# Optimization experiments

Hardware: AMD Instinct MI355X
Metric: run time of the kernel (lower is better)

The kernel has to match this reference:

```python
import jax, jax.numpy as jnp
import numpy as np

ALPHA = 0.2  # LeakyReLU negative slope
N, IN_DIM, OUT_DIM = 8192, 512, 64


def setup_inputs() -> dict:
    key = jax.random.key(0)
    k1, k2, k3, k4 = jax.random.split(key, 4)
    X = jax.random.normal(k1, (N, IN_DIM), dtype=jnp.float32)
    Adj = jax.random.randint(k2, (N, N), 0, 2, dtype=jnp.int32)
    # xavier_uniform with gain=1.414
    def xavier(k, shape, gain=1.414):
        fan_in, fan_out = shape[0], shape[1]
        bound = gain * np.sqrt(6.0 / (fan_in + fan_out))
        return jax.random.uniform(k, shape, jnp.float32, -bound, bound)
    W = xavier(k3, (IN_DIM, OUT_DIM))
    a = xavier(k4, (2 * OUT_DIM, 1))
    return {"X": X, "Adj": Adj, "W": W, "a": a}


def reference(X, Adj, W, a):
    # h = X @ W : [N, D]
    h = X @ W
    D = h.shape[1]
    # Decompose pairwise score: concat([h_i, h_j]) @ a == h_i @ a1 + h_j @ a2
    s1 = h @ a[:D, 0]   # [N] -- contribution of row (destination) node i
    s2 = h @ a[D:, 0]   # [N] -- contribution of column (source) node j
    e = jnp.exp(jax.nn.leaky_relu(s1[:, None] + s2[None, :], negative_slope=ALPHA))  # [N, N]
    e = jnp.where(Adj == 0, jnp.float32(0.0), e)
    attention = e / jnp.sum(e, axis=1, keepdims=True)
    # dropout is a no-op in eval mode (training=False)
    return attention @ h
```

## Files before the change

kernel.cpp:

```cpp
#include <hip/hip_runtime.h>
#include <math.h>


#define NN 8192
#define KIN 512
#define DD 64
#define ALPHA 0.2f

using floatx4 = __attribute__((ext_vector_type(4))) float;
using bf16x8  = __attribute__((ext_vector_type(8))) __bf16;

__global__ __launch_bounds__(256) void k_fused(const float* __restrict__ X,
                                               const float* __restrict__ W,
                                               const float* __restrict__ a,
                                               float* __restrict__ s1,
                                               float* __restrict__ s2,
                                               __bf16* __restrict__ hFrag) {
    __shared__ __align__(16) float smem[3200];
    float* XT = smem;
    float* WL = smem + 32 * 36;
    float* hT = smem;
    const int t = threadIdx.x;
    const int i0 = blockIdx.x * 32;
    const int rb = t >> 5;
    const int db = t & 31;
    float acc[4][2] = {};

    for (int k0 = 0; k0 < KIN; k0 += 32) {
        {
            const int row = t >> 3, kq = t & 7;
            const float4 x4 = *(const float4*)(X + (size_t)(i0 + row) * KIN + k0 + kq * 4);
            XT[(kq * 4 + 0) * 36 + row] = x4.x;
            XT[(kq * 4 + 1) * 36 + row] = x4.y;
            XT[(kq * 4 + 2) * 36 + row] = x4.z;
            XT[(kq * 4 + 3) * 36 + row] = x4.w;
#pragma unroll
            for (int p = 0; p < 2; ++p) {
                const int q = p * 256 + t;
                const int kk = q >> 4, dq = q & 15;
                *(float4*)(WL + kk * 64 + dq * 4) =
                    *(const float4*)(W + (size_t)(k0 + kk) * DD + dq * 4);
            }
        }
        __syncthreads();
#pragma unroll
        for (int k = 0; k < 32; ++k) {
            const float4 xa = *(const float4*)(XT + k * 36 + rb * 4);
            const float2 wb = *(const float2*)(WL + k * 64 + db * 2);
            const float xv[4] = {xa.x, xa.y, xa.z, xa.w};
#pragma unroll
            for (int i = 0; i < 4; ++i) {
                acc[i][0] += xv[i] * wb.x;
                acc[i][1] += xv[i] * wb.y;
            }
        }
        __syncthreads();
    }
#pragma unroll
    for (int i = 0; i < 4; ++i) {
        hT[(rb * 4 + i) * 66 + db * 2 + 0] = acc[i][0];
        hT[(rb * 4 + i) * 66 + db * 2 + 1] = acc[i][1];
    }
    __syncthreads();
    {
        const int r = t >> 3, sub = t & 7;
        float p1 = 0.f, p2 = 0.f;
#pragma unroll
        for (int u = 0; u < 8; ++u) {
            const int d = sub * 8 + u;
            const float v = hT[r * 66 + d];
            p1 += v * a[d];
            p2 += v * a[64 + d];
        }
#pragma unroll
        for (int off = 1; off < 8; off <<= 1) {
            p1 += __shfl_xor(p1, off, 64);
            p2 += __shfl_xor(p2, off, 64);
        }
        if (sub == 0) {
            s1[i0 + r] = p1;
            s2[i0 + r] = p2;
        }
    }
    {
        const int lane = t & 63, dt = t >> 6;
        const int n = lane & 15, q = lane >> 4;
        bf16x8 v;
#pragma unroll
        for (int jj = 0; jj < 8; ++jj)
            v[jj] = (__bf16)hT[(q * 8 + jj) * 66 + dt * 16 + n];
        *(bf16x8*)(hFrag + ((size_t)blockIdx.x * 256 + t) * 8) = v;
    }
}

__global__ __launch_bounds__(256) void k_pack(const int* __restrict__ Adj,
                                              unsigned int* __restrict__ mask) {
    const int lane = threadIdx.x & 63;
    const int wid = (blockIdx.x * 256 + threadIdx.x) >> 6;
    const int nw = (gridDim.x * 256) >> 6;
    for (int it = wid; it < (NN * NN / 512); it += nw) {
        const size_t base = (size_t)it * 512;
        unsigned long long m[8];
#pragma unroll
        for (int p = 0; p < 8; ++p) {
            const int v = Adj[base + (size_t)p * 64 + lane];
            m[p] = __ballot(v != 0);
        }
        if (lane == 0) {
            unsigned long long* o = (unsigned long long*)mask + (size_t)it * 8;
#pragma unroll
            for (int p = 0; p < 8; ++p) o[p] = m[p];
        }
    }
}

__global__ __launch_bounds__(256, 4) void k_attn5(const bf16x8* __restrict__ hFrag,
                                                  const unsigned int* __restrict__ mask,
                                                  const float* __restrict__ s1,
                                                  const float* __restrict__ s2,
                                                  float* __restrict__ numP,
                                                  float* __restrict__ denP) {
    const int t = threadIdx.x;
    const int wv = t >> 6;
    const int lane = t & 63;
    const int n = lane & 15, q = lane >> 4;
    const int it = blockIdx.x >> 3, jc = blockIdx.x & 7;
    const int i0 = it * 64;
    const int row = i0 + wv * 16 + n;
    const float s1v = s1[row];
    const unsigned int* mrow = mask + (size_t)row * 256 + jc * 32;
    const int jbase = jc * 1024;

    bf16x8 ones;
#pragma unroll
    for (int u = 0; u < 8; ++u) ones[u] = (__bf16)1.0f;

    floatx4 acc[5] = {};

#pragma unroll 1
    for (int o = 0; o < 4; ++o) {
        const uint4 mA = *(const uint4*)(mrow + o * 8);
        const uint4 mB = *(const uint4*)(mrow + o * 8 + 4);
        const unsigned int mr[8] = {mA.x, mA.y, mA.z, mA.w, mB.x, mB.y, mB.z, mB.w};
#pragma unroll
        for (int k8 = 0; k8 < 8; ++k8) {
            const int ks = o * 8 + k8;
            const int j0 = jbase + ks * 32 + q * 8;
            const float4 z0 = *(const float4*)(s2 + j0);
            const float4 z1 = *(const float4*)(s2 + j0 + 4);
            const unsigned int bits = (mr[k8] >> (q * 8)) & 0xffu;
            const float zz[8] = {z0.x, z0.y, z0.z, z0.w, z1.x, z1.y, z1.z, z1.w};
            bf16x8 af;
#pragma unroll
            for (int u = 0; u < 8; ++u) {
                const float s = s1v + zz[u];
                const float l = fmaxf(s, ALPHA * s);
                const float e = (bits & (1u << u)) ? __expf(l) : 0.f;
                af[u] = (__bf16)e;
            }
            const bf16x8* hf = hFrag + ((size_t)(jc * 32 + ks) * 4) * 64 + lane;
#pragma unroll
            for (int dt = 0; dt < 4; ++dt)
                acc[dt] = __builtin_amdgcn_mfma_f32_16x16x32_bf16(af, hf[dt * 64], acc[dt], 0, 0, 0);
            acc[4] = __builtin_amdgcn_mfma_f32_16x16x32_bf16(af, ones, acc[4], 0, 0, 0);
        }
    }

    const size_t base = (size_t)blockIdx.x * 4096;
#pragma unroll
    for (int dt = 0; dt < 4; ++dt)
#pragma unroll
        for (int r = 0; r < 4; ++r)
            numP[base + (size_t)(wv * 16 + q * 4 + r) * 64 + dt * 16 + n] = acc[dt][r];

    if (n == 0) {
#pragma unroll
        for (int r = 0; r < 4; ++r)
            denP[(size_t)blockIdx.x * 64 + wv * 16 + q * 4 + r] = acc[4][r];
    }
}

__global__ __launch_bounds__(256) void k_final(const float* __restrict__ numP,
                                               const float* __restrict__ denP,
                                               float* __restrict__ out) {
    const int idx = blockIdx.x * 256 + threadIdx.x;
    const int i = idx >> 6, d = idx & 63;
    const int it = i >> 6, r = i & 63;
    float num = 0.f, den = 0.f;
#pragma unroll
    for (int c = 0; c < 8; ++c) {
        const size_t bx = (size_t)(it * 8 + c);
        num += numP[bx * 4096 + (size_t)r * 64 + d];
        den += denP[bx * 64 + r];
    }
    out[idx] = num / den;
}

extern "C" void kernel_launch(void* const* d_in, const int* in_sizes, int n_in,
                              void* d_out, int out_size, void* d_ws, size_t ws_size,
                              hipStream_t stream) {
    const float* X = (const float*)d_in[0];
    const int* Adj = (const int*)d_in[1];
    const float* W = (const float*)d_in[2];
    const float* a = (const float*)d_in[3];
    float* out = (float*)d_out;

    float* ws = (float*)d_ws;
    float* s1 = ws;
    float* s2 = s1 + 8192;
    __bf16* hFrag = (__bf16*)(s2 + 8192);
    unsigned int* mask = (unsigned int*)(s2 + 8192 + 262144);
    float* numP = (float*)(s2 + 8192 + 262144 + 2097152);
    float* denP = numP + 1024 * 4096;

    k_fused<<<256, 256, 0, stream>>>(X, W, a, s1, s2, hFrag);
    k_pack<<<2048, 256, 0, stream>>>(Adj, mask);
    k_attn5<<<1024, 256, 0, stream>>>((const bf16x8*)hFrag, mask, s1, s2, numP, denP);
    k_final<<<2048, 256, 0, stream>>>(numP, denP, out);
}
```

Before: 445.1 us.

## Fuse adjacency mask packing into attention kernel reading Adj directly

Removes the separate bit-packing kernel and has the attention kernel load int32 adjacency entries directly with nontemporal vector loads. This avoids a kernel launch plus writing and rereading the packed mask, and lets the adjacency stream overlap with exp and MFMA work. The cost is that the attention kernel now streams the full int32 matrix with per-row strided accesses, which may be less efficiently coalesced than the packing kernel's reads.

```diff
diff --git a/kernel.cpp b/kernel.cpp
--- a/kernel.cpp
+++ b/kernel.cpp
@@ -9,6 +9,7 @@
 
 using floatx4 = __attribute__((ext_vector_type(4))) float;
 using bf16x8  = __attribute__((ext_vector_type(8))) __bf16;
+using intx4   = __attribute__((ext_vector_type(4))) int;
 
 __global__ __launch_bounds__(256) void k_fused(const float* __restrict__ X,
                                                const float* __restrict__ W,
@@ -93,29 +94,8 @@
     }
 }
 
-__global__ __launch_bounds__(256) void k_pack(const int* __restrict__ Adj,
-                                              unsigned int* __restrict__ mask) {
-    const int lane = threadIdx.x & 63;
-    const int wid = (blockIdx.x * 256 + threadIdx.x) >> 6;
-    const int nw = (gridDim.x * 256) >> 6;
-    for (int it = wid; it < (NN * NN / 512); it += nw) {
-        const size_t base = (size_t)it * 512;
-        unsigned long long m[8];
-#pragma unroll
-        for (int p = 0; p < 8; ++p) {
-            const int v = Adj[base + (size_t)p * 64 + lane];
-            m[p] = __ballot(v != 0);
-        }
-        if (lane == 0) {
-            unsigned long long* o = (unsigned long long*)mask + (size_t)it * 8;
-#pragma unroll
-            for (int p = 0; p < 8; ++p) o[p] = m[p];
-        }
-    }
-}
-
-__global__ __launch_bounds__(256, 4) void k_attn5(const bf16x8* __restrict__ hFrag,
-                                                  const unsigned int* __restrict__ mask,
+__global__ __launch_bounds__(256, 4) void k_attn6(const bf16x8* __restrict__ hFrag,
+                                                  const int* __restrict__ Adj,
                                                   const float* __restrict__ s1,
                                                   const float* __restrict__ s2,
                                                   float* __restrict__ numP,
@@ -128,8 +108,10 @@
     const int i0 = it * 64;
     const int row = i0 + wv * 16 + n;
     const float s1v = s1[row];
-    const unsigned int* mrow = mask + (size_t)row * 256 + jc * 32;
     const int jbase = jc * 1024;
+    const int* adjL = Adj + (size_t)row * NN + jbase + q * 8;
+    const float* s2L = s2 + jbase + q * 8;
+    const bf16x8* hfL = hFrag + (size_t)(jc * 32) * 4 * 64 + lane;
 
     bf16x8 ones;
 #pragma unroll
@@ -138,27 +120,32 @@
     floatx4 acc[5] = {};
 
 #pragma unroll 1
-    for (int o = 0; o < 4; ++o) {
-        const uint4 mA = *(const uint4*)(mrow + o * 8);
-        const uint4 mB = *(const uint4*)(mrow + o * 8 + 4);
-        const unsigned int mr[8] = {mA.x, mA.y, mA.z, mA.w, mB.x, mB.y, mB.z, mB.w};
-#pragma unroll
-        for (int k8 = 0; k8 < 8; ++k8) {
-            const int ks = o * 8 + k8;
-            const int j0 = jbase + ks * 32 + q * 8;
-            const float4 z0 = *(const float4*)(s2 + j0);
-            const float4 z1 = *(const float4*)(s2 + j0 + 4);
-            const unsigned int bits = (mr[k8] >> (q * 8)) & 0xffu;
-            const float zz[8] = {z0.x, z0.y, z0.z, z0.w, z1.x, z1.y, z1.z, z1.w};
+    for (int ks = 0; ks < 32; ks += 2) {
+        const intx4 a00 = __builtin_nontemporal_load((const intx4*)(adjL + ks * 32));
+        const intx4 a01 = __builtin_nontemporal_load((const intx4*)(adjL + ks * 32 + 4));
+        const intx4 a10 = __builtin_nontemporal_load((const intx4*)(adjL + ks * 32 + 32));
+        const intx4 a11 = __builtin_nontemporal_load((const intx4*)(adjL + ks * 32 + 36));
+        const float4 z00 = *(const float4*)(s2L + ks * 32);
+        const float4 z01 = *(const float4*)(s2L + ks * 32 + 4);
+        const float4 z10 = *(const float4*)(s2L + ks * 32 + 32);
+        const float4 z11 = *(const float4*)(s2L + ks * 32 + 36);
+#pragma unroll
+        for (int sub = 0; sub < 2; ++sub) {
+            const intx4 aa = sub ? a10 : a00;
+            const intx4 ab = sub ? a11 : a01;
+            const float4 za = sub ? z10 : z00;
+            const float4 zb = sub ? z11 : z01;
+            const int am[8] = {aa.x, aa.y, aa.z, aa.w, ab.x, ab.y, ab.z, ab.w};
+            const float zz[8] = {za.x, za.y, za.z, za.w, zb.x, zb.y, zb.z, zb.w};
             bf16x8 af;
 #pragma unroll
             for (int u = 0; u < 8; ++u) {
                 const float s = s1v + zz[u];
                 const float l = fmaxf(s, ALPHA * s);
-                const float e = (bits & (1u << u)) ? __expf(l) : 0.f;
+                const float e = am[u] ? __expf(l) : 0.f;
                 af[u] = (__bf16)e;
             }
-            const bf16x8* hf = hFrag + ((size_t)(jc * 32 + ks) * 4) * 64 + lane;
+            const bf16x8* hf = hfL + (size_t)(ks + sub) * 4 * 64;
 #pragma unroll
             for (int dt = 0; dt < 4; ++dt)
                 acc[dt] = __builtin_amdgcn_mfma_f32_16x16x32_bf16(af, hf[dt * 64], acc[dt], 0, 0, 0);
@@ -209,12 +196,10 @@
     float* s1 = ws;
     float* s2 = s1 + 8192;
     __bf16* hFrag = (__bf16*)(s2 + 8192);
-    unsigned int* mask = (unsigned int*)(s2 + 8192 + 262144);
-    float* numP = (float*)(s2 + 8192 + 262144 + 2097152);
+    float* numP = (float*)(s2 + 8192 + 262144);
     float* denP = numP + 1024 * 4096;
 
     k_fused<<<256, 256, 0, stream>>>(X, W, a, s1, s2, hFrag);
-    k_pack<<<2048, 256, 0, stream>>>(Adj, mask);
-    k_attn5<<<1024, 256, 0, stream>>>((const bf16x8*)hFrag, mask, s1, s2, numP, denP);
+    k_attn6<<<1024, 256, 0, stream>>>((const bf16x8*)hFrag, Adj, s1, s2, numP, denP);
     k_final<<<2048, 256, 0, stream>>>(numP, denP, out);
 }
```

New measurement: 443.0 us. No clear change (-0.5%).
